# Kernel tuning notes

Measured on AMD Instinct MI355X. Metric: run time of the kernel, lower is better.

Reference implementation:

```python
import jax, jax.numpy as jnp
import numpy as np

B, T, D = 32, 256, 512
P, V = 2048, 40000
DFF = 2148
K_CONCEPT = 50
K_PHENO = 10
EPS = 1e-6


def setup_inputs() -> dict:
    key = jax.random.key(0)
    ks = jax.random.split(key, 10)
    return {
        "visit_embeddings": jax.random.normal(ks[0], (B, T, D), jnp.float32) * 0.05,
        "visit_mask": jax.random.randint(ks[1], (B, T), 0, 2, jnp.int32),
        "embedding_matrix": jax.random.normal(ks[2], (V, D), jnp.float32) * 0.05,
        "phenotype_embeddings": jax.random.normal(ks[3], (P, D), jnp.float32) * 0.05,
        "w1": jax.random.normal(ks[4], (D, DFF), jnp.float32) * (1.0 / np.sqrt(D)),
        "b1": jnp.zeros((DFF,), jnp.float32),
        "w2": jax.random.normal(ks[5], (DFF, D), jnp.float32) * (1.0 / np.sqrt(DFF)),
        "b2": jnp.zeros((D,), jnp.float32),
        "ln1_g": jnp.ones((D,), jnp.float32),
        "ln1_b": jnp.zeros((D,), jnp.float32),
        "ln2_g": jnp.ones((D,), jnp.float32),
        "ln2_b": jnp.zeros((D,), jnp.float32),
    }


def _layer_norm(x, g, b):
    mu = jnp.mean(x, axis=-1, keepdims=True)
    var = jnp.mean(jnp.square(x - mu), axis=-1, keepdims=True)
    return (x - mu) * jax.lax.rsqrt(var + EPS) * g + b


def _smallest_k(x, k):
    # top_k of -x selects the k smallest values per row
    return -jax.lax.top_k(-x, k)[0]


def reference(visit_embeddings, visit_mask, embedding_matrix, phenotype_embeddings,
              w1, b1, w2, b2, ln1_g, ln1_b, ln2_g, ln2_b):
    # mask: original mask==1 means padded; converted mask is 1.0 for valid positions
    conv_mask = (1.0 - visit_mask.astype(jnp.float32))[:, :, None]  # [B,T,1]

    # phenotype attention: softmax over (logits * mask)  (faithful to TF code)
    logits = jnp.einsum('btd,pd->btp', visit_embeddings, phenotype_embeddings) * conv_mask
    probs = jax.nn.softmax(logits, axis=-1)  # [B,T,P]

    # phenotype-concept euclidean distance metric (cdist + row-wise smallest-k)
    r_p = jnp.sum(phenotype_embeddings * phenotype_embeddings, axis=1)[:, None]  # [P,1]
    r_c = jnp.sum(embedding_matrix * embedding_matrix, axis=1)[None, :]          # [1,V]
    d_pc = jnp.sqrt(r_p + r_c - 2.0 * phenotype_embeddings @ embedding_matrix.T)  # [P,V]
    phenotype_concept_dist = jnp.mean(_smallest_k(d_pc, K_CONCEPT))

    # phenotype probability entropy metric
    entropy = -jnp.sum(probs * jnp.log(probs) * conv_mask, axis=-1)  # [B,T]

    # phenotype-phenotype squared-distance metrics
    d_pp = r_p - 2.0 * phenotype_embeddings @ phenotype_embeddings.T + r_p.T  # [P,P]
    near = _smallest_k(d_pp, K_PHENO)  # [P,K_PHENO]
    phe_inv_loss = jnp.mean(jnp.exp(-near))
    phe_dist_metric = jnp.mean(near)
    phe_dist_var = jnp.var(near)

    # residual + FFN block (dropout is identity at inference)
    ctx = probs @ phenotype_embeddings  # [B,T,D]
    out1 = _layer_norm(visit_embeddings + ctx, ln1_g, ln1_b)
    ffn = jnp.maximum(out1 @ w1 + b1, 0.0) @ w2 + b2
    out2 = _layer_norm(out1 + ffn, ln2_g, ln2_b)

    return (out2, probs, phenotype_concept_dist, entropy,
            phe_inv_loss, phe_dist_metric, phe_dist_var)
```

## Files before the change

kernel.cpp:

```cpp
#include <hip/hip_runtime.h>
#include <stdint.h>
#include <stddef.h>

#define BATCH 32
#define TLEN 256
#define DIM 512
#define PHE 2048
#define VOC 40000
#define VOCP 40960
#define DFF 2148
#define DFFP2 2304
#define BT 8192
#define KC 50
#define KP 10
#define CHUNK 8192
#define NCHUNK 5
#define LNEPS 1e-6f
#define BIGF 1e30f

typedef unsigned short u16;
typedef __attribute__((ext_vector_type(8))) short short8;
typedef __attribute__((ext_vector_type(8))) unsigned short ushort8;
typedef __attribute__((ext_vector_type(4))) float floatx4;

__device__ inline u16 f2bf(float f) {
  union { float f; unsigned int u; } v; v.f = f;
  unsigned int u = v.u;
  return (u16)((u + 0x7fffu + ((u >> 16) & 1u)) >> 16);
}
__device__ inline float bf2f(u16 u) {
  union { unsigned int u; float f; } c; c.u = ((unsigned int)u) << 16;
  return c.f;
}

__device__ inline unsigned int f2mono(float f) {
  union { float f; unsigned int u; } c; c.f = f;
  return (c.u & 0x80000000u) ? ~c.u : (c.u | 0x80000000u);
}
__device__ inline float mono2f(unsigned int u) {
  union { unsigned int u; float f; } c;
  c.u = (u & 0x80000000u) ? (u & 0x7FFFFFFFu) : ~u;
  return c.f;
}
__device__ inline unsigned int mono16(u16 u) {
  return (u & 0x8000u) ? (u16)~u : (u16)(u | 0x8000u);
}
__device__ inline float mono2f16(unsigned int k) {
  unsigned int ub = (k & 0x8000u) ? (k & 0x7FFFu) : ((~k) & 0xFFFFu);
  union { unsigned int u; float f; } c; c.u = ub << 16;
  return c.f;
}

__device__ inline void load_lds16(const void* g, void* l) {
  __builtin_amdgcn_global_load_lds(
      (const __attribute__((address_space(1))) unsigned int*)g,
      (__attribute__((address_space(3))) unsigned int*)l, 16, 0, 0);
}

__device__ inline float waveRedSum(float v) {
  #pragma unroll
  for (int off = 32; off > 0; off >>= 1) v += __shfl_down(v, off);
  return v;
}
__device__ inline float waveRedMax(float v) {
  #pragma unroll
  for (int off = 32; off > 0; off >>= 1) v = fmaxf(v, __shfl_down(v, off));
  return v;
}
__device__ inline float blockRedSum(float v) {
  __shared__ float sm[8];
  int lane = threadIdx.x & 63, w = threadIdx.x >> 6, nw = blockDim.x >> 6;
  v = waveRedSum(v);
  __syncthreads();
  if (lane == 0) sm[w] = v;
  __syncthreads();
  float r = 0.f;
  for (int i = 0; i < nw; ++i) r += sm[i];
  return r;
}
__device__ inline float blockRedMax(float v) {
  __shared__ float sm2[8];
  int lane = threadIdx.x & 63, w = threadIdx.x >> 6, nw = blockDim.x >> 6;
  v = waveRedMax(v);
  __syncthreads();
  if (lane == 0) sm2[w] = v;
  __syncthreads();
  float r = -BIGF;
  for (int i = 0; i < nw; ++i) r = fmaxf(r, sm2[i]);
  return r;
}
__device__ inline double blockRedSumD(double v) {
  __shared__ double red[256];
  int tid = threadIdx.x;
  __syncthreads();
  red[tid] = v;
  __syncthreads();
  for (int s = 128; s > 0; s >>= 1) {
    if (tid < s) red[tid] += red[tid + s];
    __syncthreads();
  }
  return red[0];
}

__device__ inline void hist_add2(int* hist, int digit, bool pred) {
  int lane = threadIdx.x & 63;
  unsigned long long act = __ballot(pred);
  if (!act) return;
  int src = __ffsll((long long)act) - 1;
  int ld = __shfl(digit, src);
  unsigned long long m = __ballot(pred && digit == ld);
  if (__popcll(m) >= 32) {
    if (lane == src) atomicAdd(&hist[ld], (int)__popcll(m));
    if ((act & ~m) & (1ull << lane)) atomicAdd(&hist[digit], 1);
  } else {
    if (pred) atomicAdd(&hist[digit], 1);
  }
}

__global__ void k_sentinel(float* out) { out[0] = -12345.0f; }

#define PREP_VIS 2048
#define PREP_PHT 1024
#define PREP_W1  1152
#define PREP_W2  1152
__global__ void __launch_bounds__(256) k_prep(
    const float* __restrict__ emb, u16* __restrict__ emb_bf, float* __restrict__ r_c,
    const float* __restrict__ phe, u16* __restrict__ phe_bf, float* __restrict__ r_p,
    const float* __restrict__ visit, u16* __restrict__ visit_bf,
    u16* __restrict__ pheT_bf,
    const float* __restrict__ w1, u16* __restrict__ w1T_bf,
    const float* __restrict__ w2, u16* __restrict__ w2T_bf)
{
  __shared__ float tile[32][33];
  int bid = (int)blockIdx.x, tid = threadIdx.x;
  if (bid < VOC + PHE) {
    const float* src = (bid < VOC) ? emb + (size_t)bid * DIM
                                   : phe + (size_t)(bid - VOC) * DIM;
    u16* dst = (bid < VOC) ? emb_bf + (size_t)bid * DIM
                           : phe_bf + (size_t)(bid - VOC) * DIM;
    float a = src[tid], b = src[tid + 256];
    dst[tid] = f2bf(a); dst[tid + 256] = f2bf(b);
    float s = blockRedSum(a * a + b * b);
    if (tid == 0) {
      if (bid < VOC) r_c[bid] = s; else r_p[bid - VOC] = s;
    }
    return;
  }
  int b2 = bid - (VOC + PHE);
  int rr = tid >> 5, cc = tid & 31;
  if (b2 < PREP_VIS) {
    int base = b2 * 2048 + tid;
    #pragma unroll
    for (int e = 0; e < 8; ++e) {
      int i = base + e * 256;
      visit_bf[i] = f2bf(visit[i]);
    }
    return;
  }
  b2 -= PREP_VIS;
  if (b2 < PREP_PHT) {
    int i0 = (b2 >> 4) << 5, j0 = (b2 & 15) << 5;
    #pragma unroll
    for (int p = 0; p < 4; ++p)
      tile[p * 8 + rr][cc] = phe[(size_t)(i0 + p * 8 + rr) * DIM + j0 + cc];
    __syncthreads();
    #pragma unroll
    for (int p = 0; p < 4; ++p)
      pheT_bf[(size_t)(j0 + p * 8 + rr) * PHE + i0 + cc] = f2bf(tile[cc][p * 8 + rr]);
    return;
  }
  b2 -= PREP_PHT;
  if (b2 < PREP_W1) {
    int r0 = (b2 >> 4) << 5, c0 = (b2 & 15) << 5;
    #pragma unroll
    for (int p = 0; p < 4; ++p) {
      int i = p * 8 + rr;
      tile[i][cc] = (r0 + cc < DFF) ? w1[(size_t)(c0 + i) * DFF + r0 + cc] : 0.f;
    }
    __syncthreads();
    #pragma unroll
    for (int p = 0; p < 4; ++p) {
      int a = p * 8 + rr;
      w1T_bf[(size_t)(r0 + a) * DIM + c0 + cc] = f2bf(tile[cc][a]);
    }
    return;
  }
  b2 -= PREP_W1;
  {
    int r0 = (b2 / 72) << 5, c0 = (b2 % 72) << 5;
    #pragma unroll
    for (int p = 0; p < 4; ++p) {
      int i = p * 8 + rr;
      tile[i][cc] = (c0 + i < DFF) ? w2[(size_t)(c0 + i) * DIM + r0 + cc] : 0.f;
    }
    __syncthreads();
    #pragma unroll
    for (int p = 0; p < 4; ++p) {
      int a = p * 8 + rr;
      w2T_bf[(size_t)(r0 + a) * DFFP2 + c0 + cc] = f2bf(tile[cc][a]);
    }
    return;
  }
}

#define EPI_STORE 0
#define EPI_DPP   1
#define EPI_FFN1  3
#define EPI_FFN2  4

__device__ inline void xcd_block(int BM, int BN, int& m0, int& n0) {
  int nwg = gridDim.x * gridDim.y;
  int orig = blockIdx.y * gridDim.x + blockIdx.x;
  int q = nwg >> 3, r = nwg & 7;
  int xcd = orig & 7, i0 = orig >> 3;
  int wgid = (xcd < r ? xcd * (q + 1) : r * (q + 1) + (xcd - r) * q) + i0;
  m0 = (wgid / gridDim.x) * BM;
  n0 = (wgid % gridDim.x) * BN;
}

template<int EPI>
__device__ inline void epi_write(int rr, int col, float c,
    float* outF, u16* outU, int ldc, const float* rp,
    const float* bias, int nepi) {
  if (EPI == EPI_STORE) {
    outF[(size_t)rr * ldc + col] = c;
  } else if (EPI == EPI_DPP) {
    outF[(size_t)rr * ldc + col] = rp[rr] + rp[col] - 2.f * c;
  } else if (EPI == EPI_FFN1) {
    float h = (col < nepi) ? fmaxf(c + bias[col], 0.f) : 0.f;
    outU[(size_t)rr * ldc + col] = f2bf(h);
  } else if (EPI == EPI_FFN2) {
    outF[(size_t)rr * ldc + col] = c + bias[col];
  }
}

__device__ __forceinline__ void dpc_select(
    char* smem, int si, const u16* __restrict__ dr, int schunk,
    float* __restrict__ top)
{
  int row = si >> 1, half = si & 1;
  const u16* src = dr + (size_t)row * CHUNK + half * 4096;
  int* hist = (int*)smem;
  int* cum  = hist + 1024;
  int* wred = cum + 256;
  int* selb = wred + 8;
  int tid = threadIdx.x, lane = tid & 63, w4 = tid >> 6;
  int hbase = w4 << 8;

  unsigned int kv[16];
  #pragma unroll
  for (int j2 = 0; j2 < 2; ++j2) {
    ushort8 qv = *(const ushort8*)(src + j2 * 2048 + tid * 8);
    #pragma unroll
    for (int e = 0; e < 8; ++e) kv[j2 * 8 + e] = mono16((u16)qv[e]);
  }

  int hbmin = 255, hbmax = 0;
  #pragma unroll
  for (int j = 0; j < 16; ++j) {
    int hb = (int)(kv[j] >> 8);
    hbmin = min(hbmin, hb); hbmax = max(hbmax, hb);
  }
  #pragma unroll
  for (int off = 32; off > 0; off >>= 1) {
    hbmin = min(hbmin, __shfl_down(hbmin, off));
    hbmax = max(hbmax, __shfl_down(hbmax, off));
  }
  if (lane == 0) { wred[w4] = hbmin; wred[4 + w4] = hbmax; }
  __syncthreads();
  int bmin = min(min(wred[0], wred[1]), min(wred[2], wred[3]));
  int bmax = max(max(wred[4], wred[5]), max(wred[6], wred[7]));
  __syncthreads();

  unsigned int prefix;
  int kk = KC;
  if (bmin == bmax) {
    prefix = (unsigned int)bmin;
  } else {
    hist[tid] = 0; hist[tid + 256] = 0; hist[tid + 512] = 0; hist[tid + 768] = 0;
    __syncthreads();
    #pragma unroll
    for (int j = 0; j < 16; ++j) hist_add2(hist + hbase, (int)(kv[j] >> 8), true);
    __syncthreads();
    int x = hist[tid] + hist[tid + 256] + hist[tid + 512] + hist[tid + 768];
    #pragma unroll
    for (int off = 1; off < 64; off <<= 1) { int y = __shfl_up(x, off); if (lane >= off) x += y; }
    if (lane == 63) wred[w4] = x;
    __syncthreads();
    #pragma unroll
    for (int i = 0; i < 4; ++i) if (i < w4) x += wred[i];
    cum[tid] = x;
    __syncthreads();
    int prev = (tid == 0) ? 0 : cum[tid - 1];
    if (prev < kk && kk <= cum[tid]) { selb[0] = tid; selb[1] = kk - prev; }
    __syncthreads();
    prefix = (unsigned int)selb[0];
    kk = selb[1];
    __syncthreads();
  }

  hist[tid] = 0; hist[tid + 256] = 0; hist[tid + 512] = 0; hist[tid + 768] = 0;
  __syncthreads();
  #pragma unroll
  for (int j = 0; j < 16; ++j)
    hist_add2(hist + hbase, (int)(kv[j] & 255u), (kv[j] >> 8) == prefix);
  __syncthreads();
  int x = hist[tid] + hist[tid + 256] + hist[tid + 512] + hist[tid + 768];
  #pragma unroll
  for (int off = 1; off < 64; off <<= 1) { int y = __shfl_up(x, off); if (lane >= off) x += y; }
  if (lane == 63) wred[w4] = x;
  __syncthreads();
  #pragma unroll
  for (int i = 0; i < 4; ++i) if (i < w4) x += wred[i];
  cum[tid] = x;
  __syncthreads();
  int prev = (tid == 0) ? 0 : cum[tid - 1];
  if (prev < kk && kk <= cum[tid]) { selb[0] = tid; selb[1] = kk - prev; }
  __syncthreads();
  unsigned int key = (prefix << 8) | (unsigned int)selb[0];
  float thr = mono2f16(key);
  float* o50 = top + (size_t)row * (NCHUNK * 2 * KC) + (schunk * 2 + half) * KC;
  __syncthreads();

  int cless = 0;
  #pragma unroll
  for (int j = 0; j < 16; ++j) if (kv[j] < key) cless++;
  int xc = cless;
  #pragma unroll
  for (int off = 1; off < 64; off <<= 1) { int y = __shfl_up(xc, off); if (lane >= off) xc += y; }
  if (lane == 63) wred[w4] = xc;
  __syncthreads();
  #pragma unroll
  for (int i = 0; i < 4; ++i) if (i < w4) xc += wred[i];
  int o = xc - cless;
  #pragma unroll
  for (int j = 0; j < 16; ++j)
    if (kv[j] < key) o50[o++] = mono2f16(kv[j]);
  cum[tid] = xc;
  __syncthreads();
  int total_less = cum[255];
  for (int i = total_less + tid; i < KC; i += 256) o50[i] = thr;
}

__global__ void __launch_bounds__(256, 2) k_dpc(
    const u16* __restrict__ phe_bf, const u16* __restrict__ emb_bf,
    int gchunk, int ngemm, u16* __restrict__ dw,
    const u16* __restrict__ dr, int schunk, float* __restrict__ top,
    const float* __restrict__ rp, const float* __restrict__ rc)
{
  __shared__ __align__(16) char smem[32768];
  int bid = (int)blockIdx.x;
  if (bid < ngemm) {
    u16* As = (u16*)smem;
    u16* Bs = (u16*)(smem + 16384);
    int tid = threadIdx.x, lane = tid & 63, w = tid >> 6;
    int wm = w >> 1, wn = w & 1;
    int nwg = ngemm, orig = bid;
    int q = nwg >> 3, r = nwg & 7;
    int xcd = orig & 7, i0 = orig >> 3;
    int wgid = (xcd < r ? xcd * (q + 1) : r * (q + 1) + (xcd - r) * q) + i0;
    int m0 = (wgid >> 6) << 7;
    int n0 = (wgid & 63) << 7;
    const u16* Bm = emb_bf + (size_t)gchunk * CHUNK * DIM;
    const float* rcc = rc + gchunk * CHUNK;
    int bvalid = VOC - gchunk * CHUNK; if (bvalid > CHUNK) bvalid = CHUNK;

    floatx4 acc[4][4];
    #pragma unroll
    for (int i = 0; i < 4; ++i)
      #pragma unroll
      for (int j = 0; j < 4; ++j)
        acc[i][j] = (floatx4){0.f, 0.f, 0.f, 0.f};

    int hi = lane >> 4, rsw = lane & 7;
    for (int kt = 0; kt < DIM / 64; ++kt) {
      int k0 = kt * 64;
      #pragma unroll
      for (int p = 0; p < 4; ++p) {
        int c = p * 256 + tid;
        int row = c >> 3;
        int src16 = (c & 7) ^ (row & 7);
        load_lds16(phe_bf + (size_t)(m0 + row) * DIM + k0 + src16 * 8,
                   &As[p * 2048 + w * 512]);
      }
      #pragma unroll
      for (int p = 0; p < 4; ++p) {
        int c = p * 256 + tid;
        int row = c >> 3;
        int src16 = (c & 7) ^ (row & 7);
        load_lds16(Bm + (size_t)(n0 + row) * DIM + k0 + src16 * 8,
                   &Bs[p * 2048 + w * 512]);
      }
      __syncthreads();
      #pragma unroll
      for (int ks = 0; ks < 2; ++ks) {
        int chk = ((ks << 2) | hi) ^ rsw;
        short8 a[4], b[4];
        #pragma unroll
        for (int i = 0; i < 4; ++i)
          a[i] = *(const short8*)&As[(wm * 64 + i * 16 + (lane & 15)) * 64 + chk * 8];
        #pragma unroll
        for (int j = 0; j < 4; ++j)
          b[j] = *(const short8*)&Bs[(wn * 64 + j * 16 + (lane & 15)) * 64 + chk * 8];
        #pragma unroll
        for (int i = 0; i < 4; ++i)
          #pragma unroll
          for (int j = 0; j < 4; ++j)
            acc[i][j] = __builtin_amdgcn_mfma_f32_16x16x32_bf16(a[i], b[j], acc[i][j], 0, 0, 0);
      }
      __syncthreads();
    }
    #pragma unroll
    for (int i = 0; i < 4; ++i) {
      #pragma unroll
      for (int j = 0; j < 4; ++j) {
        floatx4 v = acc[i][j];
        int col = n0 + wn * 64 + j * 16 + (lane & 15);
        int rb = m0 + wm * 64 + i * 16 + ((lane >> 4) << 2);
        #pragma unroll
        for (int qq = 0; qq < 4; ++qq) {
          int rr = rb + qq;
          float d = (col < bvalid) ? sqrtf(fmaxf(rp[rr] + rcc[col] - 2.f * v[qq], 0.f)) : BIGF;
          dw[(size_t)rr * CHUNK + col] = f2bf(d);
        }
      }
    }
  } else {
    if (schunk < 0) return;
    dpc_select(smem, bid - ngemm, dr, schunk, top);
  }
}

__global__ void __launch_bounds__(256, 2) k_dpc_log(
    const u16* __restrict__ visit_bf, const u16* __restrict__ phe_bf,
    int ngemm, u16* __restrict__ logit_bf,
    const u16* __restrict__ dr, int schunk, float* __restrict__ top)
{
  __shared__ __align__(16) char smem[32768];
  int bid = (int)blockIdx.x;
  if (bid < ngemm) {
    u16* As = (u16*)smem;
    u16* Bs = (u16*)(smem + 16384);
    int tid = threadIdx.x, lane = tid & 63, w = tid >> 6;
    int wm = w >> 1, wn = w & 1;
    int nwg = ngemm, orig = bid;
    int q = nwg >> 3, r = nwg & 7;
    int xcd = orig & 7, i0 = orig >> 3;
    int wgid = (xcd < r ? xcd * (q + 1) : r * (q + 1) + (xcd - r) * q) + i0;
    int m0 = (wgid >> 4) << 7;
    int n0 = (wgid & 15) << 7;

    floatx4 acc[4][4];
    #pragma unroll
    for (int i = 0; i < 4; ++i)
      #pragma unroll
      for (int j = 0; j < 4; ++j)
        acc[i][j] = (floatx4){0.f, 0.f, 0.f, 0.f};

    int hi = lane >> 4, rsw = lane & 7;
    for (int kt = 0; kt < DIM / 64; ++kt) {
      int k0 = kt * 64;
      #pragma unroll
      for (int p = 0; p < 4; ++p) {
        int c = p * 256 + tid;
        int row = c >> 3;
        int src16 = (c & 7) ^ (row & 7);
        load_lds16(visit_bf + (size_t)(m0 + row) * DIM + k0 + src16 * 8,
                   &As[p * 2048 + w * 512]);
      }
      #pragma unroll
      for (int p = 0; p < 4; ++p) {
        int c = p * 256 + tid;
        int row = c >> 3;
        int src16 = (c & 7) ^ (row & 7);
        load_lds16(phe_bf + (size_t)(n0 + row) * DIM + k0 + src16 * 8,
                   &Bs[p * 2048 + w * 512]);
      }
      __syncthreads();
      #pragma unroll
      for (int ks = 0; ks < 2; ++ks) {
        int chk = ((ks << 2) | hi) ^ rsw;
        short8 a[4], b[4];
        #pragma unroll
        for (int i = 0; i < 4; ++i)
          a[i] = *(const short8*)&As[(wm * 64 + i * 16 + (lane & 15)) * 64 + chk * 8];
        #pragma unroll
        for (int j = 0; j < 4; ++j)
          b[j] = *(const short8*)&Bs[(wn * 64 + j * 16 + (lane & 15)) * 64 + chk * 8];
        #pragma unroll
        for (int i = 0; i < 4; ++i)
          #pragma unroll
          for (int j = 0; j < 4; ++j)
            acc[i][j] = __builtin_amdgcn_mfma_f32_16x16x32_bf16(a[i], b[j], acc[i][j], 0, 0, 0);
      }
      __syncthreads();
    }
    #pragma unroll
    for (int i = 0; i < 4; ++i) {
      #pragma unroll
      for (int j = 0; j < 4; ++j) {
        floatx4 v = acc[i][j];
        int col = n0 + wn * 64 + j * 16 + (lane & 15);
        int rb = m0 + wm * 64 + i * 16 + ((lane >> 4) << 2);
        #pragma unroll
        for (int qq = 0; qq < 4; ++qq)
          logit_bf[(size_t)(rb + qq) * PHE + col] = f2bf(v[qq]);
      }
    }
  } else {
    if (schunk < 0) return;
    dpc_select(smem, bid - ngemm, dr, schunk, top);
  }
}

template<int EPI, int BM, int BN, int NTH, int WR, int WC>
__global__ void __launch_bounds__(NTH, 2) k_gemm2(
    const u16* __restrict__ A, int lda,
    const u16* __restrict__ Bm, int ldb, int K,
    float* __restrict__ outF, u16* __restrict__ outU, int ldc,
    const float* __restrict__ rp, const float* __restrict__ bias, int nepi)
{
  constexpr int BK = 64;
  constexpr int MR = BM / WR / 16;
  constexpr int NR = BN / WC / 16;
  constexpr int LD_A = BM * BK / (NTH * 8);
  constexpr int LD_B = BN * BK / (NTH * 8);
  __shared__ __align__(16) u16 As[2][BM * BK];
  __shared__ __align__(16) u16 Bs[2][BN * BK];
  int tid = threadIdx.x, lane = tid & 63, w = tid >> 6;
  int wm = w / WC, wn = w % WC;
  int m0, n0;
  xcd_block(BM, BN, m0, n0);

  floatx4 acc[MR][NR];
  #pragma unroll
  for (int i = 0; i < MR; ++i)
    #pragma unroll
    for (int j = 0; j < NR; ++j)
      acc[i][j] = (floatx4){0.f, 0.f, 0.f, 0.f};

  auto stage = [&](int buf, int k0) {
    #pragma unroll
    for (int p = 0; p < LD_A; ++p) {
      int c = p * NTH + tid;
      int row = c >> 3;
      int src16 = (c & 7) ^ (row & 7);
      load_lds16(A + (size_t)(m0 + row) * lda + k0 + src16 * 8,
                 &As[buf][p * NTH * 8 + w * 512]);
    }
    #pragma unroll
    for (int p = 0; p < LD_B; ++p) {
      int c = p * NTH + tid;
      int row = c >> 3;
      int src16 = (c & 7) ^ (row & 7);
      load_lds16(Bm + (size_t)(n0 + row) * ldb + k0 + src16 * 8,
                 &Bs[buf][p * NTH * 8 + w * 512]);
    }
  };

  int nt = K / BK;
  stage(0, 0);
  __syncthreads();
  int cur = 0;
  int hi = lane >> 4;
  int rsw = lane & 7;
  for (int kt = 0; kt < nt; ++kt) {
    if (kt + 1 < nt) stage(cur ^ 1, (kt + 1) * BK);
    #pragma unroll
    for (int ks = 0; ks < 2; ++ks) {
      int chk = ((ks << 2) | hi) ^ rsw;
      short8 a[MR], b[NR];
      #pragma unroll
      for (int i = 0; i < MR; ++i)
        a[i] = *(const short8*)&As[cur][(wm * (BM / WR) + i * 16 + (lane & 15)) * BK + chk * 8];
      #pragma unroll
      for (int j = 0; j < NR; ++j)
        b[j] = *(const short8*)&Bs[cur][(wn * (BN / WC) + j * 16 + (lane & 15)) * BK + chk * 8];
      #pragma unroll
      for (int i = 0; i < MR; ++i)
        #pragma unroll
        for (int j = 0; j < NR; ++j)
          acc[i][j] = __builtin_amdgcn_mfma_f32_16x16x32_bf16(a[i], b[j], acc[i][j], 0, 0, 0);
    }
    __syncthreads();
    cur ^= 1;
  }

  #pragma unroll
  for (int i = 0; i < MR; ++i) {
    #pragma unroll
    for (int j = 0; j < NR; ++j) {
      floatx4 v = acc[i][j];
      int col = n0 + wn * (BN / WC) + j * 16 + (lane & 15);
      int rb = m0 + wm * (BM / WR) + i * 16 + ((lane >> 4) << 2);
      #pragma unroll
      for (int qq = 0; qq < 4; ++qq)
        epi_write<EPI>(rb + qq, col, v[qq], outF, outU, ldc, rp, bias, nepi);
    }
  }
}

template<int EPI>
__global__ void __launch_bounds__(256, 4) k_gemm2s(
    const u16* __restrict__ A, int lda,
    const u16* __restrict__ Bm, int ldb, int K,
    float* __restrict__ outF, u16* __restrict__ outU, int ldc,
    const float* __restrict__ rp, const float* __restrict__ bias, int nepi)
{
  constexpr int BM = 128, BN = 128, BK = 64, NTH = 256;
  constexpr int MR = 4, NR = 4;
  __shared__ __align__(16) u16 As[BM * BK];
  __shared__ __align__(16) u16 Bs[BN * BK];
  int tid = threadIdx.x, lane = tid & 63, w = tid >> 6;
  int wm = w >> 1, wn = w & 1;
  int m0, n0;
  xcd_block(BM, BN, m0, n0);

  floatx4 acc[MR][NR];
  #pragma unroll
  for (int i = 0; i < MR; ++i)
    #pragma unroll
    for (int j = 0; j < NR; ++j)
      acc[i][j] = (floatx4){0.f, 0.f, 0.f, 0.f};

  int hi = lane >> 4;
  int rsw = lane & 7;
  int nt = K / BK;
  for (int kt = 0; kt < nt; ++kt) {
    int k0 = kt * BK;
    #pragma unroll
    for (int p = 0; p < 4; ++p) {
      int c = p * NTH + tid;
      int row = c >> 3;
      int src16 = (c & 7) ^ (row & 7);
      load_lds16(A + (size_t)(m0 + row) * lda + k0 + src16 * 8,
                 &As[p * NTH * 8 + w * 512]);
    }
    #pragma unroll
    for (int p = 0; p < 4; ++p) {
      int c = p * NTH + tid;
      int row = c >> 3;
      int src16 = (c & 7) ^ (row & 7);
      load_lds16(Bm + (size_t)(n0 + row) * ldb + k0 + src16 * 8,
                 &Bs[p * NTH * 8 + w * 512]);
    }
    __syncthreads();
    #pragma unroll
    for (int ks = 0; ks < 2; ++ks) {
      int chk = ((ks << 2) | hi) ^ rsw;
      short8 a[MR], b[NR];
      #pragma unroll
      for (int i = 0; i < MR; ++i)
        a[i] = *(const short8*)&As[(wm * 64 + i * 16 + (lane & 15)) * BK + chk * 8];
      #pragma unroll
      for (int j = 0; j < NR; ++j)
        b[j] = *(const short8*)&Bs[(wn * 64 + j * 16 + (lane & 15)) * BK + chk * 8];
      #pragma unroll
      for (int i = 0; i < MR; ++i)
        #pragma unroll
        for (int j = 0; j < NR; ++j)
          acc[i][j] = __builtin_amdgcn_mfma_f32_16x16x32_bf16(a[i], b[j], acc[i][j], 0, 0, 0);
    }
    __syncthreads();
  }

  #pragma unroll
  for (int i = 0; i < MR; ++i) {
    #pragma unroll
    for (int j = 0; j < NR; ++j) {
      floatx4 v = acc[i][j];
      int col = n0 + wn * 64 + j * 16 + (lane & 15);
      int rb = m0 + wm * 64 + i * 16 + ((lane >> 4) << 2);
      #pragma unroll
      for (int qq = 0; qq < 4; ++qq)
        epi_write<EPI>(rb + qq, col, v[qq], outF, outU, ldc, rp, bias, nepi);
    }
  }
}

__global__ void __launch_bounds__(256) k_softmax(
    u16* __restrict__ probs_bf, const int* __restrict__ mask,
    float* __restrict__ probs, float* __restrict__ entropy)
{
  int row = blockIdx.x;
  int tid = threadIdx.x;
  u16* pb = probs_bf + (size_t)row * PHE;
  float* pp = probs + (size_t)row * PHE;
  if (mask[row] != 0) {
    const float u = 1.0f / (float)PHE;
    const u16 ub = f2bf(u);
    for (int i = tid; i < PHE; i += 256) { pp[i] = u; pb[i] = ub; }
    if (tid == 0) entropy[row] = 0.f;
    return;
  }
  float l[8];
  float mx = -BIGF;
  #pragma unroll
  for (int j = 0; j < 8; ++j) { l[j] = bf2f(pb[tid + j * 256]); mx = fmaxf(mx, l[j]); }
  mx = blockRedMax(mx);
  float s = 0.f;
  #pragma unroll
  for (int j = 0; j < 8; ++j) { l[j] = __expf(l[j] - mx); s += l[j]; }
  s = blockRedSum(s);
  float inv = 1.0f / s;
  float ent = 0.f;
  #pragma unroll
  for (int j = 0; j < 8; ++j) {
    float p = l[j] * inv;
    pp[tid + j * 256] = p;
    pb[tid + j * 256] = f2bf(p);
    ent += p * __logf(p);
  }
  ent = blockRedSum(ent);
  if (tid == 0) entropy[row] = -ent;
}

__global__ void __launch_bounds__(256) k_ln(
    const float* __restrict__ xa, const float* __restrict__ xb,
    const float* __restrict__ g, const float* __restrict__ bb,
    float* __restrict__ outF, u16* __restrict__ outBf)
{
  int row = blockIdx.x;
  int tid = threadIdx.x;
  const float* pa = xa + (size_t)row * DIM;
  const float* pb = xb + (size_t)row * DIM;
  float x0 = pa[tid] + pb[tid];
  float x1 = pa[tid + 256] + pb[tid + 256];
  float mu = blockRedSum(x0 + x1) * (1.0f / DIM);
  float d0 = x0 - mu, d1 = x1 - mu;
  float var = blockRedSum(d0 * d0 + d1 * d1) * (1.0f / DIM);
  float rs = 1.0f / sqrtf(var + LNEPS);
  float y0 = d0 * rs * g[tid] + bb[tid];
  float y1 = d1 * rs * g[tid + 256] + bb[tid + 256];
  if (outF) {
    outF[(size_t)row * DIM + tid] = y0;
    outF[(size_t)row * DIM + tid + 256] = y1;
  }
  if (outBf) {
    outBf[(size_t)row * DIM + tid] = f2bf(y0);
    outBf[(size_t)row * DIM + tid + 256] = f2bf(y1);
  }
}

template<int NPER>
__global__ void __launch_bounds__(256) k_rsel(
    const float* __restrict__ in, int ldin, int ncols, int k, int mode,
    float* __restrict__ out)
{
  __shared__ int hist[1024];
  __shared__ int cum[256];
  __shared__ int wsum[4];
  __shared__ int sel_bucket, sel_rank;
  int row = blockIdx.x;
  int tid = threadIdx.x;
  int lane = tid & 63, w = tid >> 6;
  int hbase = w << 8;
  const float* src = in + (size_t)row * ldin;

  unsigned int v[NPER];
  #pragma unroll
  for (int j = 0; j < NPER; ++j) {
    int idx = tid + j * 256;
    v[j] = (idx < ncols) ? f2mono(src[idx]) : 0xFFFFFFFFu;
  }

  unsigned int prefix = 0, pmask = 0;
  int kk = k;
  for (int shift = 24; shift >= 0; shift -= 8) {
    hist[tid] = 0; hist[tid + 256] = 0; hist[tid + 512] = 0; hist[tid + 768] = 0;
    __syncthreads();
    #pragma unroll
    for (int j = 0; j < NPER; ++j)
      hist_add2(hist + hbase, (int)((v[j] >> shift) & 255), (v[j] & pmask) == prefix);
    __syncthreads();
    int x = hist[tid] + hist[tid + 256] + hist[tid + 512] + hist[tid + 768];
    #pragma unroll
    for (int off = 1; off < 64; off <<= 1) {
      int y = __shfl_up(x, off);
      if (lane >= off) x += y;
    }
    if (lane == 63) wsum[w] = x;
    __syncthreads();
    #pragma unroll
    for (int i = 0; i < 4; ++i) if (i < w) x += wsum[i];
    cum[tid] = x;
    __syncthreads();
    int prev = (tid == 0) ? 0 : cum[tid - 1];
    if (prev < kk && kk <= cum[tid]) { sel_bucket = tid; sel_rank = kk - prev; }
    __syncthreads();
    prefix |= ((unsigned int)sel_bucket) << shift;
    pmask |= 255u << shift;
    kk = sel_rank;
    __syncthreads();
  }

  float thr = mono2f(prefix);
  int need = kk;

  float s = 0.f, se = 0.f, sq = 0.f;
  #pragma unroll
  for (int j = 0; j < NPER; ++j) {
    if (v[j] < prefix) {
      float f = mono2f(v[j]);
      s += f; se += __expf(-f); sq += f * f;
    }
  }
  float ts = blockRedSum(s);
  float tse = blockRedSum(se);
  float tsq = blockRedSum(sq);
  if (tid == 0) {
    float fn = (float)need;
    ts += fn * thr;
    if (mode == 1) {
      out[row] = ts;
    } else {
      tse += fn * __expf(-thr);
      tsq += fn * thr * thr;
      out[(size_t)row * 4] = ts;
      out[(size_t)row * 4 + 1] = tse;
      out[(size_t)row * 4 + 2] = tsq;
    }
  }
}

__global__ void __launch_bounds__(256) k_final(
    const float* __restrict__ row_sum50, const float* __restrict__ pp_part,
    float* __restrict__ out_pcd, float* __restrict__ out_inv,
    float* __restrict__ out_mean, float* __restrict__ out_var)
{
  int tid = threadIdx.x;
  double s50 = 0, sn = 0, se = 0, sq = 0;
  for (int i = tid; i < PHE; i += 256) {
    s50 += (double)row_sum50[i];
    sn += (double)pp_part[(size_t)i * 4];
    se += (double)pp_part[(size_t)i * 4 + 1];
    sq += (double)pp_part[(size_t)i * 4 + 2];
  }
  s50 = blockRedSumD(s50);
  sn = blockRedSumD(sn);
  se = blockRedSumD(se);
  sq = blockRedSumD(sq);
  if (tid == 0) {
    *out_pcd = (float)(s50 / (double)(PHE * KC));
    double mean = sn / (double)(PHE * KP);
    *out_inv = (float)(se / (double)(PHE * KP));
    *out_mean = (float)mean;
    *out_var = (float)(sq / (double)(PHE * KP) - mean * mean);
  }
}

extern "C" void kernel_launch(void* const* d_in, const int* in_sizes, int n_in,
                              void* d_out, int out_size, void* d_ws, size_t ws_size,
                              hipStream_t stream)
{
  const float* visit = (const float*)d_in[0];
  const int*   vmask = (const int*)d_in[1];
  const float* emb   = (const float*)d_in[2];
  const float* phe   = (const float*)d_in[3];
  const float* w1    = (const float*)d_in[4];
  const float* b1    = (const float*)d_in[5];
  const float* w2    = (const float*)d_in[6];
  const float* b2    = (const float*)d_in[7];
  const float* ln1g  = (const float*)d_in[8];
  const float* ln1b  = (const float*)d_in[9];
  const float* ln2g  = (const float*)d_in[10];
  const float* ln2b  = (const float*)d_in[11];

  float* out = (float*)d_out;
  float* out2      = out;
  float* probs     = out + (size_t)BT * DIM;
  float* pcd       = probs + (size_t)BT * PHE;
  float* entropy   = pcd + 1;
  float* inv_loss  = entropy + BT;
  float* dist_mean = inv_loss + 1;
  float* dist_var  = dist_mean + 1;

  char* wsb = (char*)d_ws;
  size_t off = 0;
  auto alloc = [&](size_t bytes) -> char* {
    char* p = wsb + off;
    off = (off + bytes + 255) & ~(size_t)255;
    return p;
  };
  u16* phe_bf   = (u16*)alloc((size_t)PHE * DIM * 2);
  u16* pheT_bf  = (u16*)alloc((size_t)DIM * PHE * 2);
  u16* visit_bf = (u16*)alloc((size_t)BT * DIM * 2);
  u16* w1T_bf   = (u16*)alloc((size_t)DFFP2 * DIM * 2);
  u16* w2T_bf   = (u16*)alloc((size_t)DIM * DFFP2 * 2);
  float* r_p    = (float*)alloc((size_t)PHE * 4);
  float* r_c    = (float*)alloc((size_t)VOC * 4);
  char* big1    = alloc((size_t)67108864);
  char* big2    = alloc((size_t)VOCP * DIM * 2);
  float* top50c = (float*)alloc((size_t)PHE * NCHUNK * 2 * KC * 4);
  char* big3    = alloc((size_t)PHE * PHE * 4);
  u16* probs_bf = (u16*)alloc((size_t)BT * PHE * 2);
  float* out1_f = (float*)alloc((size_t)BT * DIM * 4);
  u16* out1_bf  = (u16*)alloc((size_t)BT * DIM * 2);
  float* ffn_f  = (float*)alloc((size_t)BT * DIM * 4);
  float* row_sum50 = (float*)alloc((size_t)PHE * 4);
  float* pp_part   = (float*)alloc((size_t)PHE * 4 * 4);

  u16* dchunk0  = (u16*)big1;
  u16* dchunk1  = (u16*)(big1 + 33554432);
  u16* emb_bf   = (u16*)big2;
  u16* h_bf     = (u16*)big2;
  float* d_pp   = (float*)big3;
  float* ctx_f  = (float*)big3;

  if (ws_size < off) { k_sentinel<<<1, 1, 0, stream>>>(out); return; }

  int nprep = (VOC + PHE) + PREP_VIS + PREP_PHT + PREP_W1 + PREP_W2;
  k_prep<<<nprep, 256, 0, stream>>>(emb, emb_bf, r_c, phe, phe_bf, r_p,
                                    visit, visit_bf, pheT_bf, w1, w1T_bf, w2, w2T_bf);

  for (int c = 0; c < NCHUNK; ++c) {
    int s = c - 1;
    int nsel = (s >= 0) ? PHE * 2 : 0;
    u16* dw = (c & 1) ? dchunk1 : dchunk0;
    const u16* dr = (s >= 0) ? ((s & 1) ? dchunk1 : dchunk0) : nullptr;
    k_dpc<<<1024 + nsel, 256, 0, stream>>>(
        phe_bf, emb_bf, c, 1024, dw, dr, s, top50c, r_p, r_c);
  }
  k_dpc_log<<<1024 + PHE * 2, 256, 0, stream>>>(
      visit_bf, phe_bf, 1024, probs_bf,
      (NCHUNK - 1) & 1 ? dchunk1 : dchunk0, NCHUNK - 1, top50c);
  k_rsel<2><<<PHE, 256, 0, stream>>>(top50c, NCHUNK * 2 * KC, NCHUNK * 2 * KC, KC, 1, row_sum50);

  k_gemm2<EPI_DPP, 128, 128, 256, 2, 2><<<dim3(PHE / 128, PHE / 128), 256, 0, stream>>>(
      phe_bf, DIM, phe_bf, DIM, DIM, d_pp, nullptr, PHE, r_p, nullptr, 0);
  k_rsel<8><<<PHE, 256, 0, stream>>>(d_pp, PHE, PHE, KP, 2, pp_part);

  k_softmax<<<BT, 256, 0, stream>>>(probs_bf, vmask, probs, entropy);
  k_gemm2<EPI_STORE, 64, 128, 256, 2, 2><<<dim3(DIM / 128, BT / 64), 256, 0, stream>>>(
      probs_bf, PHE, pheT_bf, PHE, PHE, ctx_f, nullptr, DIM, nullptr, nullptr, 0);

  k_ln<<<BT, 256, 0, stream>>>(visit, ctx_f, ln1g, ln1b, out1_f, out1_bf);
  k_gemm2s<EPI_FFN1><<<dim3(DFFP2 / 128, BT / 128), 256, 0, stream>>>(
      out1_bf, DIM, w1T_bf, DIM, DIM, nullptr, h_bf, DFFP2, nullptr, b1, DFF);
  k_gemm2<EPI_FFN2, 64, 128, 256, 2, 2><<<dim3(DIM / 128, BT / 64), 256, 0, stream>>>(
      h_bf, DFFP2, w2T_bf, DFFP2, DFFP2, ffn_f, nullptr, DIM, nullptr, b2, 0);
  k_ln<<<BT, 256, 0, stream>>>(out1_f, ffn_f, ln2g, ln2b, out2, nullptr);

  k_final<<<1, 256, 0, stream>>>(row_sum50, pp_part, pcd, inv_loss, dist_mean, dist_var);
}
```

Baseline: 564.9 us.

## Fold phenotype-distance GEMM and top-k select into the d_pc chunk launches

```diff
diff --git a/kernel.cpp b/kernel.cpp
--- a/kernel.cpp
+++ b/kernel.cpp
@@ -342,18 +342,21 @@
   for (int i = total_less + tid; i < KC; i += 256) o50[i] = thr;
 }
 
+template<int NDPPG, int NDPPS>
 __global__ void __launch_bounds__(256, 2) k_dpc(
     const u16* __restrict__ phe_bf, const u16* __restrict__ emb_bf,
     int gchunk, int ngemm, u16* __restrict__ dw,
     const u16* __restrict__ dr, int schunk, float* __restrict__ top,
-    const float* __restrict__ rp, const float* __restrict__ rc)
+    const float* __restrict__ rp, const float* __restrict__ rc, int nsel,
+    float* __restrict__ d_pp, float* __restrict__ pp_part)
 {
   __shared__ __align__(16) char smem[32768];
   int bid = (int)blockIdx.x;
+  int tid = threadIdx.x;
   if (bid < ngemm) {
     u16* As = (u16*)smem;
     u16* Bs = (u16*)(smem + 16384);
-    int tid = threadIdx.x, lane = tid & 63, w = tid >> 6;
+    int lane = tid & 63, w = tid >> 6;
     int wm = w >> 1, wn = w & 1;
     int nwg = ngemm, orig = bid;
     int q = nwg >> 3, r = nwg & 7;
@@ -425,9 +428,152 @@
         }
       }
     }
-  } else {
-    if (schunk < 0) return;
-    dpc_select(smem, bid - ngemm, dr, schunk, top);
+    return;
+  }
+  bid -= ngemm;
+  if (NDPPG > 0) {
+    if (bid < NDPPG) {
+      u16* As = (u16*)smem;
+      u16* Bs = (u16*)(smem + 16384);
+      int lane = tid & 63, w = tid >> 6;
+      int wm = w >> 1, wn = w & 1;
+      int m0 = (bid >> 4) << 7;
+      int n0 = (bid & 15) << 7;
+
+      floatx4 acc[4][4];
+      #pragma unroll
+      for (int i = 0; i < 4; ++i)
+        #pragma unroll
+        for (int j = 0; j < 4; ++j)
+          acc[i][j] = (floatx4){0.f, 0.f, 0.f, 0.f};
+
+      int hi = lane >> 4, rsw = lane & 7;
+      for (int kt = 0; kt < DIM / 64; ++kt) {
+        int k0 = kt * 64;
+        #pragma unroll
+        for (int p = 0; p < 4; ++p) {
+          int c = p * 256 + tid;
+          int row = c >> 3;
+          int src16 = (c & 7) ^ (row & 7);
+          load_lds16(phe_bf + (size_t)(m0 + row) * DIM + k0 + src16 * 8,
+                     &As[p * 2048 + w * 512]);
+        }
+        #pragma unroll
+        for (int p = 0; p < 4; ++p) {
+          int c = p * 256 + tid;
+          int row = c >> 3;
+          int src16 = (c & 7) ^ (row & 7);
+          load_lds16(phe_bf + (size_t)(n0 + row) * DIM + k0 + src16 * 8,
+                     &Bs[p * 2048 + w * 512]);
+        }
+        __syncthreads();
+        #pragma unroll
+        for (int ks = 0; ks < 2; ++ks) {
+          int chk = ((ks << 2) | hi) ^ rsw;
+          short8 a[4], b[4];
+          #pragma unroll
+          for (int i = 0; i < 4; ++i)
+            a[i] = *(const short8*)&As[(wm * 64 + i * 16 + (lane & 15)) * 64 + chk * 8];
+          #pragma unroll
+          for (int j = 0; j < 4; ++j)
+            b[j] = *(const short8*)&Bs[(wn * 64 + j * 16 + (lane & 15)) * 64 + chk * 8];
+          #pragma unroll
+          for (int i = 0; i < 4; ++i)
+            #pragma unroll
+            for (int j = 0; j < 4; ++j)
+              acc[i][j] = __builtin_amdgcn_mfma_f32_16x16x32_bf16(a[i], b[j], acc[i][j], 0, 0, 0);
+        }
+        __syncthreads();
+      }
+      #pragma unroll
+      for (int i = 0; i < 4; ++i) {
+        #pragma unroll
+        for (int j = 0; j < 4; ++j) {
+          floatx4 v = acc[i][j];
+          int col = n0 + wn * 64 + j * 16 + (lane & 15);
+          int rb = m0 + wm * 64 + i * 16 + ((lane >> 4) << 2);
+          #pragma unroll
+          for (int qq = 0; qq < 4; ++qq) {
+            int rr = rb + qq;
+            d_pp[(size_t)rr * PHE + col] = rp[rr] + rp[col] - 2.f * v[qq];
+          }
+        }
+      }
+      return;
+    }
+    bid -= NDPPG;
+  }
+  if (bid < nsel) {
+    if (schunk >= 0) dpc_select(smem, bid, dr, schunk, top);
+    return;
+  }
+  bid -= nsel;
+  if (NDPPS > 0) {
+    if (bid >= NDPPS) return;
+    int row = bid;
+    const float* src = d_pp + (size_t)row * PHE;
+    int* hist = (int*)smem;
+    int* cum  = hist + 1024;
+    int* wsum = cum + 256;
+    int* selb = wsum + 4;
+    float* fred = (float*)(selb + 2);
+    int lane = tid & 63, w4 = tid >> 6;
+    int hbase = w4 << 8;
+
+    unsigned int v[8];
+    #pragma unroll
+    for (int j = 0; j < 8; ++j) v[j] = f2mono(src[tid + j * 256]);
+
+    unsigned int prefix = 0, pmask = 0;
+    int kk = KP;
+    for (int shift = 24; shift >= 0; shift -= 8) {
+      hist[tid] = 0; hist[tid + 256] = 0; hist[tid + 512] = 0; hist[tid + 768] = 0;
+      __syncthreads();
+      #pragma unroll
+      for (int j = 0; j < 8; ++j)
+        hist_add2(hist + hbase, (int)((v[j] >> shift) & 255), (v[j] & pmask) == prefix);
+      __syncthreads();
+      int x = hist[tid] + hist[tid + 256] + hist[tid + 512] + hist[tid + 768];
+      #pragma unroll
+      for (int off = 1; off < 64; off <<= 1) { int y = __shfl_up(x, off); if (lane >= off) x += y; }
+      if (lane == 63) wsum[w4] = x;
+      __syncthreads();
+      #pragma unroll
+      for (int i = 0; i < 4; ++i) if (i < w4) x += wsum[i];
+      cum[tid] = x;
+      __syncthreads();
+      int prev = (tid == 0) ? 0 : cum[tid - 1];
+      if (prev < kk && kk <= cum[tid]) { selb[0] = tid; selb[1] = kk - prev; }
+      __syncthreads();
+      prefix |= ((unsigned int)selb[0]) << shift;
+      pmask |= 255u << shift;
+      kk = selb[1];
+      __syncthreads();
+    }
+
+    float thr = mono2f(prefix);
+    int need = kk;
+    float s = 0.f, se = 0.f, sq = 0.f;
+    #pragma unroll
+    for (int j = 0; j < 8; ++j) {
+      if (v[j] < prefix) {
+        float f = mono2f(v[j]);
+        s += f; se += __expf(-f); sq += f * f;
+      }
+    }
+    s = waveRedSum(s); se = waveRedSum(se); sq = waveRedSum(sq);
+    if (lane == 0) { fred[w4] = s; fred[4 + w4] = se; fred[8 + w4] = sq; }
+    __syncthreads();
+    if (tid == 0) {
+      float ts = fred[0] + fred[1] + fred[2] + fred[3];
+      float tse = fred[4] + fred[5] + fred[6] + fred[7];
+      float tsq = fred[8] + fred[9] + fred[10] + fred[11];
+      float fn = (float)need;
+      pp_part[(size_t)row * 4] = ts + fn * thr;
+      pp_part[(size_t)row * 4 + 1] = tse + fn * __expf(-thr);
+      pp_part[(size_t)row * 4 + 2] = tsq + fn * thr * thr;
+    }
+    return;
   }
 }
 
@@ -913,22 +1059,24 @@
   k_prep<<<nprep, 256, 0, stream>>>(emb, emb_bf, r_c, phe, phe_bf, r_p,
                                     visit, visit_bf, pheT_bf, w1, w1T_bf, w2, w2T_bf);
 
-  for (int c = 0; c < NCHUNK; ++c) {
+  k_dpc<256, 0><<<1024 + 256, 256, 0, stream>>>(
+      phe_bf, emb_bf, 0, 1024, dchunk0, nullptr, -1, top50c, r_p, r_c, 0,
+      d_pp, pp_part);
+  k_dpc<0, 2048><<<1024 + 4096 + 2048, 256, 0, stream>>>(
+      phe_bf, emb_bf, 1, 1024, dchunk1, dchunk0, 0, top50c, r_p, r_c, 4096,
+      d_pp, pp_part);
+  for (int c = 2; c < NCHUNK; ++c) {
     int s = c - 1;
-    int nsel = (s >= 0) ? PHE * 2 : 0;
     u16* dw = (c & 1) ? dchunk1 : dchunk0;
-    const u16* dr = (s >= 0) ? ((s & 1) ? dchunk1 : dchunk0) : nullptr;
-    k_dpc<<<1024 + nsel, 256, 0, stream>>>(
-        phe_bf, emb_bf, c, 1024, dw, dr, s, top50c, r_p, r_c);
+    const u16* dr = (s & 1) ? dchunk1 : dchunk0;
+    k_dpc<0, 0><<<1024 + 4096, 256, 0, stream>>>(
+        phe_bf, emb_bf, c, 1024, dw, dr, s, top50c, r_p, r_c, 4096,
+        d_pp, pp_part);
   }
   k_dpc_log<<<1024 + PHE * 2, 256, 0, stream>>>(
       visit_bf, phe_bf, 1024, probs_bf,
       (NCHUNK - 1) & 1 ? dchunk1 : dchunk0, NCHUNK - 1, top50c);
   k_rsel<2><<<PHE, 256, 0, stream>>>(top50c, NCHUNK * 2 * KC, NCHUNK * 2 * KC, KC, 1, row_sum50);
-
-  k_gemm2<EPI_DPP, 128, 128, 256, 2, 2><<<dim3(PHE / 128, PHE / 128), 256, 0, stream>>>(
-      phe_bf, DIM, phe_bf, DIM, DIM, d_pp, nullptr, PHE, r_p, nullptr, 0);
-  k_rsel<8><<<PHE, 256, 0, stream>>>(d_pp, PHE, PHE, KP, 2, pp_part);
 
   k_softmax<<<BT, 256, 0, stream>>>(probs_bf, vmask, probs, entropy);
   k_gemm2<EPI_STORE, 64, 128, 256, 2, 2><<<dim3(DIM / 128, BT / 64), 256, 0, stream>>>(
```

Result: no change. 563.0 us (-0.3%).
